# Performance work log

Measured on AMD Instinct MI355X. Metric: run time of the kernel, lower is better.

The kernel has to match this reference:

```python
import jax, jax.numpy as jnp
import numpy as np

N, E, F, H, L, STEPS, VH = 50000, 800000, 64, 64, 4, 4, 64
S1 = H * L + H          # 320
VIN = S1 + H            # 384
REG_IN = S1 + VH + 1    # 385
EPS = 1e-5


def setup_inputs() -> dict:
    key = jax.random.key(0)
    ks = iter(jax.random.split(key, 64))
    nk = lambda: next(ks)

    def w(shape):
        fan_in = shape[-2] if len(shape) > 1 else shape[-1]
        return jax.random.normal(nk(), shape, jnp.float32) / np.float32(np.sqrt(fan_in))

    def b(shape):
        return 0.01 * jax.random.normal(nk(), shape, jnp.float32)

    return {
        "x": jax.random.normal(nk(), (N, F), jnp.float32),
        "edge_index": jax.random.randint(nk(), (2, E), 0, N, jnp.int32),
        "W_in": w((F, H)), "b_in": b((H,)),
        # stacked per-layer SAGEConv params (all layers are H->H)
        "sage_Wl": w((L, H, H)), "sage_bl": b((L, H)), "sage_Wr": w((L, H, H)),
        "bn_gamma": jnp.ones((L, H), jnp.float32) + 0.1 * jax.random.normal(nk(), (L, H), jnp.float32),
        "bn_beta": b((L, H)),
        "bn_mean": 0.1 * jax.random.normal(nk(), (L, H), jnp.float32),
        "bn_var": 1.0 + 0.5 * jax.random.uniform(nk(), (L, H), jnp.float32),
        "vW_l": w((VIN, VH)), "vb_l": b((VH,)), "vW_r": w((VIN, VH)),
        "vbn_gamma": jnp.ones((VH,), jnp.float32) + 0.1 * jax.random.normal(nk(), (VH,), jnp.float32),
        "vbn_beta": b((VH,)),
        "vbn_mean": 0.1 * jax.random.normal(nk(), (VH,), jnp.float32),
        "vbn_var": 1.0 + 0.5 * jax.random.uniform(nk(), (VH,), jnp.float32),
        "W_mu": w((VH, VH)), "b_mu": b((VH,)),
        "W_lv": w((VH, VH)), "b_lv": b((VH,)),
        "rank_W1": w((VH, H)), "rank_b1": b((H,)),
        "rank_W2": w((H, 1)), "rank_b2": b((1,)),
        "reg_W1": w((REG_IN, H)), "reg_b1": b((H,)),
        "reg_W2": w((H, H // 2)), "reg_b2": b((H // 2,)),
        "reg_W3": w((H // 2, 1)), "reg_b3": b((1,)),
    }


def reference(x, edge_index, W_in, b_in, sage_Wl, sage_bl, sage_Wr,
              bn_gamma, bn_beta, bn_mean, bn_var,
              vW_l, vb_l, vW_r, vbn_gamma, vbn_beta, vbn_mean, vbn_var,
              W_mu, b_mu, W_lv, b_lv,
              rank_W1, rank_b1, rank_W2, rank_b2,
              reg_W1, reg_b1, reg_W2, reg_b2, reg_W3, reg_b3):
    n = x.shape[0]
    row, col = edge_index[0], edge_index[1]
    ones_e = jnp.ones(row.shape, x.dtype)

    def sage(h, Wl, bl, Wr):
        # mean aggregation of source features at destination nodes (PyG SAGEConv)
        agg = jax.ops.segment_sum(h[row], col, num_segments=n)          # [N, Fin]
        cnt = jax.ops.segment_sum(ones_e, col, num_segments=n)          # in-degree
        mean = agg / jnp.maximum(cnt, 1.0)[:, None]
        return mean @ Wl + bl + h @ Wr

    def bn(h, g, be, m, v):
        return (h - m) * jax.lax.rsqrt(v + EPS) * g + be

    inp_skip = x @ W_in + b_in
    h = x
    layer_outputs = []
    for i in range(L):  # fixed small layer loop; res_proj is Identity (in_feats == hidden)
        h_fwd = jax.nn.relu(bn(sage(h, sage_Wl[i], sage_bl[i], sage_Wr[i]),
                               bn_gamma[i], bn_beta[i], bn_mean[i], bn_var[i]))
        h = h_fwd + h
        layer_outputs.append(h)
    stage1 = jnp.concatenate(layer_outputs + [inp_skip], axis=1)        # [N, 320]

    # path_agg: row-degree-normalized scatter, iterated path_steps times
    deg = jnp.maximum(jax.ops.segment_sum(ones_e, row, num_segments=n), 1.0)
    norm = (1.0 / deg)[row]                                             # [E]
    out = h
    for _ in range(STEPS):
        out = jax.ops.segment_sum(out[row] * norm[:, None], col, num_segments=n)

    vgae_in = jnp.concatenate([stage1, out], axis=1)                    # [N, 384]
    v = jax.nn.relu(bn(sage(vgae_in, vW_l, vb_l, vW_r),
                       vbn_gamma, vbn_beta, vbn_mean, vbn_var))
    mu = v @ W_mu + b_mu
    logvar = v @ W_lv + b_lv
    z = mu  # eval mode: no reparameterization noise

    rank_score = (jax.nn.relu(z @ rank_W1 + rank_b1) @ rank_W2 + rank_b2)[:, 0]

    reg_in = jnp.concatenate([stage1, z, rank_score[:, None]], axis=1)  # [N, 385]
    h1 = jax.nn.relu(reg_in @ reg_W1 + reg_b1)
    h2 = jax.nn.relu(h1 @ reg_W2 + reg_b2)
    preds = h2 @ reg_W3 + reg_b3
    return preds, rank_score, mu, logvar
```

## Files before the change

### kernel.cpp

```cpp
#include <hip/hip_runtime.h>
#include <cstdint>
#include <cstddef>

#define NN 50000
#define EE 800000
#define CAP 64
#define EPS_BN 1e-5f

typedef short  s16x8 __attribute__((ext_vector_type(8)));
typedef ushort u16x8 __attribute__((ext_vector_type(8)));
typedef float  f32x4 __attribute__((ext_vector_type(4)));

#define MFMA16(a, b, c) __builtin_amdgcn_mfma_f32_16x16x32_bf16((a), (b), (c), 0, 0, 0)

__device__ inline ushort f2bf(float f){
  uint32_t u = __float_as_uint(f);
  uint32_t r = (u + 0x7FFFu + ((u >> 16) & 1u)) >> 16;
  return (ushort)r;
}
__device__ inline float bf2f(ushort u){ return __uint_as_float((uint32_t)u << 16); }


__global__ void k_outdeg(const int* __restrict__ row, int* __restrict__ outdeg){
  int e = blockIdx.x * blockDim.x + threadIdx.x;
  if (e < EE) atomicAdd(&outdeg[row[e]], 1);
}

__global__ void k_fill(const int* __restrict__ row, const int* __restrict__ col,
                       const int* __restrict__ outdeg,
                       int* __restrict__ incnt, int* __restrict__ bsrc,
                       float* __restrict__ bnorm){
  int e = blockIdx.x * blockDim.x + threadIdx.x;
  if (e >= EE) return;
  int r = row[e], c = col[e];
  int j = atomicAdd(&incnt[c], 1);
  if (j < CAP){
    bsrc[(size_t)c * CAP + j]  = r;
    bnorm[(size_t)c * CAP + j] = 1.0f / fmaxf((float)outdeg[r], 1.0f);
  }
}


__global__ void k_cvt(const float* __restrict__ src, ushort* __restrict__ dst, int n4){
  int i = blockIdx.x * blockDim.x + threadIdx.x;
  int stride = gridDim.x * blockDim.x;
  for (; i < n4; i += stride){
    float4 v = ((const float4*)src)[i];
    ushort4 u = {f2bf(v.x), f2bf(v.y), f2bf(v.z), f2bf(v.w)};
    ((ushort4*)dst)[i] = u;
  }
}


struct FJob { const float* srcA; const float* srcB; ushort* dst;
              int NF; int NCT; int P; int mode; int splitVal; };
struct FJobs { FJob j[10]; };

__global__ void k_conv(FJobs J){
  FJob jb = J.j[blockIdx.x];
  int total = jb.NCT * jb.P * 1024;
  for (int idx = threadIdx.x + blockIdx.y * 256; idx < total; idx += 256 * gridDim.y){
    int j = idx & 7, lane = (idx >> 3) & 63, ks = (idx >> 9) & 1;
    int rest = idx >> 10;
    int p = rest % jb.P, ct = rest / jb.P;
    int col = ct * 16 + (lane & 15);
    int k   = p * 64 + ks * 32 + (lane >> 4) * 8 + j;
    const float* s = jb.srcA;
    int sc = col, sk = k;
    if (jb.mode == 1 && k   >= jb.splitVal){ s = jb.srcB; sk = k   - jb.splitVal; }
    if (jb.mode == 2 && col >= jb.splitVal){ s = jb.srcB; sc = col - jb.splitVal; }
    jb.dst[idx] = f2bf(s[(size_t)sk * jb.NF + sc]);
  }
}


__global__ void __launch_bounds__(256) k_agg(const ushort* __restrict__ hin,
                                             ushort* __restrict__ out,
                                             const int* __restrict__ bsrc,
                                             const float* __restrict__ bnorm,
                                             const int* __restrict__ incnt,
                                             int use_norm){
  __shared__ int   sidx[4][CAP];
  __shared__ float swgt[4][CAP];
  int wib  = threadIdx.x >> 6;
  int lane = threadIdx.x & 63;
  int wid  = blockIdx.x * 4 + wib;
  bool valid = wid < NN;
  int cnt  = valid ? incnt[wid] : 0;
  int cntb = min(cnt, CAP);
  if (valid){
    int   si = (lane < cntb) ? bsrc[(size_t)wid * CAP + lane] : 0;
    float wv;
    if (use_norm) wv = (lane < cntb) ? bnorm[(size_t)wid * CAP + lane] : 0.f;
    else          wv = (lane < cntb) ? 1.0f / fmaxf((float)cnt, 1.f) : 0.f;
    sidx[wib][lane] = si;
    swgt[wib][lane] = wv;
  }
  __syncthreads();
  if (!valid) return;

  int g  = lane >> 3;
  int fl = lane & 7;
  float accf[8] = {0,0,0,0,0,0,0,0};
  for (int e0 = 0; e0 < cntb; e0 += 8){
    int e = e0 + g;
    int   s = sidx[wib][e];
    float w = swgt[wib][e];
    u16x8 v = *(const u16x8*)(hin + (size_t)s * 64 + fl * 8);
    #pragma unroll
    for (int j = 0; j < 8; ++j) accf[j] = fmaf(w, bf2f(v[j]), accf[j]);
  }
  #pragma unroll
  for (int m = 8; m < 64; m <<= 1){
    #pragma unroll
    for (int j = 0; j < 8; ++j) accf[j] += __shfl_xor(accf[j], m);
  }
  if (lane < 8){
    u16x8 o;
    #pragma unroll
    for (int j = 0; j < 8; ++j) o[j] = f2bf(accf[j]);
    *(u16x8*)(out + (size_t)wid * 64 + lane * 8) = o;
  }
}


template<int P, int NCT>
__device__ inline void gemm_direct(const ushort* const* pieces,
                                   const ushort* __restrict__ WB,
                                   int rowbase, f32x4* acc){
  int lane = threadIdx.x & 63;
  int q = lane >> 4, r16 = lane & 15;
  int ar = rowbase + r16; ar = (ar < NN) ? ar : (NN - 1);
  const ushort* wl = WB + lane * 8;
  #pragma unroll
  for (int p = 0; p < P; ++p){
    const ushort* src = pieces[p] + (size_t)ar * 64 + q * 8;
    #pragma unroll
    for (int ks = 0; ks < 2; ++ks){
      s16x8 a = *(const s16x8*)(src + ks * 32);
      #pragma unroll
      for (int ct = 0; ct < NCT; ++ct){
        s16x8 b = *(const s16x8*)(wl + (((ct * P + p) * 2 + ks) << 9));
        acc[ct] = MFMA16(a, b, acc[ct]);
      }
    }
  }
}

__global__ void __launch_bounds__(256) k_skip(const ushort* __restrict__ xb,
                                              const ushort* __restrict__ WT,
                                              const float* __restrict__ bias,
                                              ushort* __restrict__ outb){
  int lane = threadIdx.x & 63, wv = threadIdx.x >> 6, q = lane >> 4, r16 = lane & 15;
  int rowbase = blockIdx.x * 64 + wv * 16;
  const ushort* pieces[1] = {xb};
  f32x4 acc[4] = {};
  gemm_direct<1, 4>(pieces, WT, rowbase, acc);
  #pragma unroll
  for (int ct = 0; ct < 4; ++ct){
    int col = ct * 16 + r16;
    float b = bias[col];
    #pragma unroll
    for (int r = 0; r < 4; ++r){
      int row = rowbase + q * 4 + r;
      if (row < NN) outb[(size_t)row * 64 + col] = f2bf(acc[ct][r] + b);
    }
  }
}

__global__ void __launch_bounds__(256) k_sage_m(const ushort* __restrict__ meanb,
                                                const ushort* __restrict__ hb,
                                                const ushort* __restrict__ WT,
                                                const float* __restrict__ bl,
                                                const float* __restrict__ g,
                                                const float* __restrict__ be,
                                                const float* __restrict__ m_,
                                                const float* __restrict__ var_,
                                                ushort* __restrict__ houtb){
  int lane = threadIdx.x & 63, wv = threadIdx.x >> 6, q = lane >> 4, r16 = lane & 15;
  int rowbase = blockIdx.x * 64 + wv * 16;
  const ushort* pieces[2] = {meanb, hb};
  f32x4 acc[4] = {};
  gemm_direct<2, 4>(pieces, WT, rowbase, acc);
  #pragma unroll
  for (int ct = 0; ct < 4; ++ct){
    int col = ct * 16 + r16;
    float sc = g[col] * rsqrtf(var_[col] + EPS_BN);
    float sh = be[col] - m_[col] * sc;
    float bb = bl[col];
    #pragma unroll
    for (int r = 0; r < 4; ++r){
      int row = rowbase + q * 4 + r;
      if (row < NN){
        float t = (acc[ct][r] + bb) * sc + sh;
        float hv = bf2f(hb[(size_t)row * 64 + col]);
        houtb[(size_t)row * 64 + col] = f2bf(fmaxf(t, 0.f) + hv);
      }
    }
  }
}

__global__ void __launch_bounds__(256) k_yr(const ushort* __restrict__ x0, const ushort* __restrict__ x1,
                                            const ushort* __restrict__ x2, const ushort* __restrict__ x3,
                                            const ushort* __restrict__ x4, const ushort* __restrict__ x5,
                                            const ushort* __restrict__ WT, const float* __restrict__ vbl,
                                            ushort* __restrict__ Y, ushort* __restrict__ R){
  int lane = threadIdx.x & 63, wv = threadIdx.x >> 6, q = lane >> 4, r16 = lane & 15;
  int rowbase = blockIdx.x * 64 + wv * 16;
  const ushort* pieces[6] = {x0, x1, x2, x3, x4, x5};
  f32x4 acc[8] = {};
  gemm_direct<6, 8>(pieces, WT, rowbase, acc);
  #pragma unroll
  for (int ct = 0; ct < 8; ++ct){
    int col = ct * 16 + r16;
    bool isR = col >= 64;
    int c2 = isR ? (col - 64) : col;
    float b = isR ? vbl[c2] : 0.f;
    ushort* dst = isR ? R : Y;
    #pragma unroll
    for (int r = 0; r < 4; ++r){
      int row = rowbase + q * 4 + r;
      if (row < NN) dst[(size_t)row * 64 + c2] = f2bf(acc[ct][r] + b);
    }
  }
}

__global__ void __launch_bounds__(256) k_mulv_m(const ushort* __restrict__ Yagg,
                                                const ushort* __restrict__ Rb,
                                                const float* __restrict__ vg,
                                                const float* __restrict__ vbe,
                                                const float* __restrict__ vm,
                                                const float* __restrict__ vvar,
                                                const ushort* __restrict__ WT,
                                                const float* __restrict__ bmu,
                                                const float* __restrict__ blv,
                                                float* __restrict__ muf, float* __restrict__ lvf,
                                                ushort* __restrict__ mub){
  __shared__ float ssc[64], ssh[64];
  int t = threadIdx.x;
  if (t < 64){
    float sc = vg[t] * rsqrtf(vvar[t] + EPS_BN);
    ssc[t] = sc; ssh[t] = vbe[t] - vm[t] * sc;
  }
  __syncthreads();
  int lane = t & 63, wv = t >> 6, q = lane >> 4, r16 = lane & 15;
  int rowbase = blockIdx.x * 64 + wv * 16;
  int ar = rowbase + r16; ar = (ar < NN) ? ar : (NN - 1);
  const ushort* wl = WT + lane * 8;
  f32x4 acc[8] = {};
  #pragma unroll
  for (int ks = 0; ks < 2; ++ks){
    int k0 = ks * 32 + q * 8;
    u16x8 y  = *(const u16x8*)(Yagg + (size_t)ar * 64 + k0);
    u16x8 rv = *(const u16x8*)(Rb   + (size_t)ar * 64 + k0);
    s16x8 a;
    #pragma unroll
    for (int j = 0; j < 8; ++j){
      float tv = (bf2f(y[j]) + bf2f(rv[j])) * ssc[k0 + j] + ssh[k0 + j];
      a[j] = (short)f2bf(fmaxf(tv, 0.f));
    }
    #pragma unroll
    for (int ct = 0; ct < 8; ++ct){
      s16x8 b = *(const s16x8*)(wl + (((ct * 1) * 2 + ks) << 9));
      acc[ct] = MFMA16(a, b, acc[ct]);
    }
  }
  #pragma unroll
  for (int ct = 0; ct < 8; ++ct){
    int col = ct * 16 + r16;
    bool isL = col >= 64;
    int c2 = isL ? (col - 64) : col;
    float bb = isL ? blv[c2] : bmu[c2];
    #pragma unroll
    for (int r = 0; r < 4; ++r){
      int row = rowbase + q * 4 + r;
      if (row < NN){
        float v = acc[ct][r] + bb;
        if (isL) lvf[(size_t)row * 64 + c2] = v;
        else { muf[(size_t)row * 64 + c2] = v; mub[(size_t)row * 64 + c2] = f2bf(v); }
      }
    }
  }
}

__global__ void __launch_bounds__(256) k_rank_m(const ushort* __restrict__ mub,
                                                const ushort* __restrict__ WT,
                                                const float* __restrict__ rb1,
                                                const float* __restrict__ rW2,
                                                const float* __restrict__ rb2,
                                                float* __restrict__ rout){
  int lane = threadIdx.x & 63, wv = threadIdx.x >> 6, q = lane >> 4, r16 = lane & 15;
  int rowbase = blockIdx.x * 64 + wv * 16;
  const ushort* pieces[1] = {mub};
  f32x4 acc[4] = {};
  gemm_direct<1, 4>(pieces, WT, rowbase, acc);
  float val[4] = {0.f, 0.f, 0.f, 0.f};
  #pragma unroll
  for (int ct = 0; ct < 4; ++ct){
    int col = ct * 16 + r16;
    float b1 = rb1[col], w2 = rW2[col];
    #pragma unroll
    for (int r = 0; r < 4; ++r)
      val[r] += fmaxf(acc[ct][r] + b1, 0.f) * w2;
  }
  #pragma unroll
  for (int r = 0; r < 4; ++r){
    #pragma unroll
    for (int m = 1; m < 16; m <<= 1) val[r] += __shfl_xor(val[r], m);
  }
  if (r16 == 0){
    float b2 = rb2[0];
    #pragma unroll
    for (int r = 0; r < 4; ++r){
      int row = rowbase + q * 4 + r;
      if (row < NN) rout[row] = val[r] + b2;
    }
  }
}

__global__ void __launch_bounds__(256) k_reg1(const ushort* __restrict__ x0, const ushort* __restrict__ x1,
                                              const ushort* __restrict__ x2, const ushort* __restrict__ x3,
                                              const ushort* __restrict__ x4, const ushort* __restrict__ x5,
                                              const float* __restrict__ rank,
                                              const ushort* __restrict__ WT,
                                              const float* __restrict__ gW1,
                                              const float* __restrict__ gb1,
                                              ushort* __restrict__ h1b){
  int lane = threadIdx.x & 63, wv = threadIdx.x >> 6, q = lane >> 4, r16 = lane & 15;
  int rowbase = blockIdx.x * 64 + wv * 16;
  const ushort* pieces[6] = {x0, x1, x2, x3, x4, x5};
  f32x4 acc[4] = {};
  gemm_direct<6, 4>(pieces, WT, rowbase, acc);
  float rk[4];
  #pragma unroll
  for (int r = 0; r < 4; ++r){
    int row = rowbase + q * 4 + r;
    rk[r] = (row < NN) ? rank[row] : 0.f;
  }
  #pragma unroll
  for (int ct = 0; ct < 4; ++ct){
    int col = ct * 16 + r16;
    float b1 = gb1[col];
    float w384 = gW1[384 * 64 + col];
    #pragma unroll
    for (int r = 0; r < 4; ++r){
      int row = rowbase + q * 4 + r;
      if (row < NN)
        h1b[(size_t)row * 64 + col] = f2bf(fmaxf(acc[ct][r] + b1 + rk[r] * w384, 0.f));
    }
  }
}

__global__ void __launch_bounds__(256) k_reg2(const ushort* __restrict__ h1b,
                                              const ushort* __restrict__ WT,
                                              const float* __restrict__ gb2,
                                              const float* __restrict__ gW3,
                                              const float* __restrict__ gb3,
                                              float* __restrict__ preds){
  int lane = threadIdx.x & 63, wv = threadIdx.x >> 6, q = lane >> 4, r16 = lane & 15;
  int rowbase = blockIdx.x * 64 + wv * 16;
  const ushort* pieces[1] = {h1b};
  f32x4 acc[2] = {};
  gemm_direct<1, 2>(pieces, WT, rowbase, acc);
  float val[4] = {0.f, 0.f, 0.f, 0.f};
  #pragma unroll
  for (int ct = 0; ct < 2; ++ct){
    int col = ct * 16 + r16;
    float b2 = gb2[col], w3 = gW3[col];
    #pragma unroll
    for (int r = 0; r < 4; ++r)
      val[r] += fmaxf(acc[ct][r] + b2, 0.f) * w3;
  }
  #pragma unroll
  for (int r = 0; r < 4; ++r){
    #pragma unroll
    for (int m = 1; m < 16; m <<= 1) val[r] += __shfl_xor(val[r], m);
  }
  if (r16 == 0){
    float b3 = gb3[0];
    #pragma unroll
    for (int r = 0; r < 4; ++r){
      int row = rowbase + q * 4 + r;
      if (row < NN) preds[row] = val[r] + b3;
    }
  }
}


extern "C" void kernel_launch(void* const* d_in, const int* in_sizes, int n_in,
                              void* d_out, int out_size, void* d_ws, size_t ws_size,
                              hipStream_t stream){
  const float* x    = (const float*)d_in[0];
  const int*   eidx = (const int*)d_in[1];
  const int* row = eidx;
  const int* col = eidx + EE;
  const float* W_in = (const float*)d_in[2];
  const float* b_in = (const float*)d_in[3];
  const float* sWl  = (const float*)d_in[4];
  const float* sbl  = (const float*)d_in[5];
  const float* sWr  = (const float*)d_in[6];
  const float* bng  = (const float*)d_in[7];
  const float* bnb  = (const float*)d_in[8];
  const float* bnm  = (const float*)d_in[9];
  const float* bnv  = (const float*)d_in[10];
  const float* vWl  = (const float*)d_in[11];
  const float* vbl  = (const float*)d_in[12];
  const float* vWr  = (const float*)d_in[13];
  const float* vg   = (const float*)d_in[14];
  const float* vbe  = (const float*)d_in[15];
  const float* vm   = (const float*)d_in[16];
  const float* vvar = (const float*)d_in[17];
  const float* Wmu  = (const float*)d_in[18];
  const float* bmu  = (const float*)d_in[19];
  const float* Wlv  = (const float*)d_in[20];
  const float* blv  = (const float*)d_in[21];
  const float* rW1  = (const float*)d_in[22];
  const float* rb1  = (const float*)d_in[23];
  const float* rW2  = (const float*)d_in[24];
  const float* rb2  = (const float*)d_in[25];
  const float* gW1  = (const float*)d_in[26];
  const float* gb1  = (const float*)d_in[27];
  const float* gW2  = (const float*)d_in[28];
  const float* gb2  = (const float*)d_in[29];
  const float* gW3  = (const float*)d_in[30];
  const float* gb3  = (const float*)d_in[31];

  float* preds = (float*)d_out;
  float* rank  = preds + NN;
  float* mu    = rank + NN;
  float* lv    = mu + (size_t)NN * 64;

  char* w = (char*)d_ws;
  auto alloc = [&](size_t bytes) -> char* {
    char* p = w; w += (bytes + 255) & ~(size_t)255; return p;
  };
  int*   outdeg = (int*)alloc((size_t)NN * 4);
  int*   incnt  = (int*)alloc((size_t)NN * 4);
  int*   bsrc   = (int*)alloc((size_t)NN * CAP * 4);
  float* bnorm  = (float*)alloc((size_t)NN * CAP * 4);
  const size_t FB = (size_t)NN * 64 * 2;
  ushort* xb    = (ushort*)alloc(FB);
  ushort* skipb = (ushort*)alloc(FB);
  ushort* hb[4];
  for (int i = 0; i < 4; ++i) hb[i] = (ushort*)alloc(FB);
  ushort* meanb = (ushort*)alloc(FB);
  ushort* pa    = (ushort*)alloc(FB);
  ushort* pb    = (ushort*)alloc(FB);
  ushort* Yb    = (ushort*)alloc(FB);
  ushort* Rb    = (ushort*)alloc(FB);
  ushort* mub   = (ushort*)alloc(FB);
  ushort* skipW = (ushort*)alloc(4 * 1024 * 2);
  ushort* sageW = (ushort*)alloc(4 * 8 * 1024 * 2);
  ushort* yrW   = (ushort*)alloc(48 * 1024 * 2);
  ushort* mulvW = (ushort*)alloc(8 * 1024 * 2);
  ushort* rankW = (ushort*)alloc(4 * 1024 * 2);
  ushort* regW1 = (ushort*)alloc(24 * 1024 * 2);
  ushort* regW2 = (ushort*)alloc(2 * 1024 * 2);

  hipMemsetAsync(outdeg, 0, (size_t)NN * 4, stream);
  hipMemsetAsync(incnt,  0, (size_t)NN * 4, stream);

  const int EB = (EE + 255) / 256;
  k_outdeg<<<EB, 256, 0, stream>>>(row, outdeg);
  k_fill  <<<EB, 256, 0, stream>>>(row, col, outdeg, incnt, bsrc, bnorm);

  FJobs J;
  auto job = [&](int i, const float* sA, const float* sB, ushort* d,
                 int NF, int NCT, int P, int mode, int splitVal){
    J.j[i] = {sA, sB, d, NF, NCT, P, mode, splitVal};
  };
  job(0, W_in, nullptr, skipW, 64, 4, 1, 0, 0);
  for (int i = 0; i < 4; ++i)
    job(1 + i, sWl + i * 4096, sWr + i * 4096, sageW + i * 8192, 64, 4, 2, 1, 64);
  job(5, vWl, vWr, yrW,   64, 8, 6, 2, 64);
  job(6, Wmu, Wlv, mulvW, 64, 8, 1, 2, 64);
  job(7, rW1, nullptr, rankW, 64, 4, 1, 0, 0);
  job(8, gW1, nullptr, regW1, 64, 4, 6, 0, 0);
  job(9, gW2, nullptr, regW2, 32, 2, 1, 0, 0);
  k_conv<<<dim3(10, 8), 256, 0, stream>>>(J);

  k_cvt<<<1024, 256, 0, stream>>>(x, xb, NN * 64 / 4);

  const int GB = (NN + 63) / 64;
  k_skip<<<GB, 256, 0, stream>>>(xb, skipW, b_in, skipb);

  const int AGG_B = (NN + 3) / 4;
  const ushort* hprev = xb;
  for (int i = 0; i < 4; ++i){
    k_agg<<<AGG_B, 256, 0, stream>>>(hprev, meanb, bsrc, bnorm, incnt, 0);
    k_sage_m<<<GB, 256, 0, stream>>>(meanb, hprev, sageW + i * 8192, sbl + i * 64,
                                     bng + i * 64, bnb + i * 64, bnm + i * 64, bnv + i * 64, hb[i]);
    hprev = hb[i];
  }

  k_agg<<<AGG_B, 256, 0, stream>>>(hb[3], pa, bsrc, bnorm, incnt, 1);
  k_agg<<<AGG_B, 256, 0, stream>>>(pa, pb, bsrc, bnorm, incnt, 1);
  k_agg<<<AGG_B, 256, 0, stream>>>(pb, pa, bsrc, bnorm, incnt, 1);
  k_agg<<<AGG_B, 256, 0, stream>>>(pa, pb, bsrc, bnorm, incnt, 1);

  k_yr<<<GB, 256, 0, stream>>>(hb[0], hb[1], hb[2], hb[3], skipb, pb, yrW, vbl, Yb, Rb);
  k_agg<<<AGG_B, 256, 0, stream>>>(Yb, meanb, bsrc, bnorm, incnt, 0);
  k_mulv_m<<<GB, 256, 0, stream>>>(meanb, Rb, vg, vbe, vm, vvar, mulvW, bmu, blv, mu, lv, mub);
  k_rank_m<<<GB, 256, 0, stream>>>(mub, rankW, rb1, rW2, rb2, rank);
  k_reg1<<<GB, 256, 0, stream>>>(hb[0], hb[1], hb[2], hb[3], skipb, mub, rank,
                                 regW1, gW1, gb1, pa);
  k_reg2<<<GB, 256, 0, stream>>>(pa, regW2, gb2, gW3, gb3, preds);
}
```

Measured before the change: 539.2 us.

## Pack edge source and degree into one word; aggregate four nodes per wave

Edge buckets now store source index and out-degree packed in one 32-bit word instead of separate index and norm arrays, halving bucket metadata traffic; weights are recomputed from the packed degree. The aggregation kernel processes four destination nodes per wave with interleaved gathers, raising memory-level parallelism and removing the block barrier. It risks wasted work when neighbor counts differ within a group and relies on indices and degrees fitting in 16 bits.

```diff
diff --git a/kernel.cpp b/kernel.cpp
--- a/kernel.cpp
+++ b/kernel.cpp
@@ -28,16 +28,13 @@
 
 __global__ void k_fill(const int* __restrict__ row, const int* __restrict__ col,
                        const int* __restrict__ outdeg,
-                       int* __restrict__ incnt, int* __restrict__ bsrc,
-                       float* __restrict__ bnorm){
+                       int* __restrict__ incnt, uint* __restrict__ bpack){
   int e = blockIdx.x * blockDim.x + threadIdx.x;
   if (e >= EE) return;
   int r = row[e], c = col[e];
   int j = atomicAdd(&incnt[c], 1);
-  if (j < CAP){
-    bsrc[(size_t)c * CAP + j]  = r;
-    bnorm[(size_t)c * CAP + j] = 1.0f / fmaxf((float)outdeg[r], 1.0f);
-  }
+  if (j < CAP)
+    bpack[(size_t)c * CAP + j] = ((uint)outdeg[r] << 16) | (uint)r;
 }
 
 
@@ -76,50 +73,67 @@
 
 __global__ void __launch_bounds__(256) k_agg(const ushort* __restrict__ hin,
                                              ushort* __restrict__ out,
-                                             const int* __restrict__ bsrc,
-                                             const float* __restrict__ bnorm,
+                                             const uint* __restrict__ bpack,
                                              const int* __restrict__ incnt,
                                              int use_norm){
-  __shared__ int   sidx[4][CAP];
-  __shared__ float swgt[4][CAP];
+  __shared__ int   ssrc[4][4][CAP];
+  __shared__ float swgt[4][4][CAP];
   int wib  = threadIdx.x >> 6;
   int lane = threadIdx.x & 63;
-  int wid  = blockIdx.x * 4 + wib;
-  bool valid = wid < NN;
-  int cnt  = valid ? incnt[wid] : 0;
-  int cntb = min(cnt, CAP);
-  if (valid){
-    int   si = (lane < cntb) ? bsrc[(size_t)wid * CAP + lane] : 0;
-    float wv;
-    if (use_norm) wv = (lane < cntb) ? bnorm[(size_t)wid * CAP + lane] : 0.f;
-    else          wv = (lane < cntb) ? 1.0f / fmaxf((float)cnt, 1.f) : 0.f;
-    sidx[wib][lane] = si;
-    swgt[wib][lane] = wv;
-  }
-  __syncthreads();
-  if (!valid) return;
-
-  int g  = lane >> 3;
-  int fl = lane & 7;
-  float accf[8] = {0,0,0,0,0,0,0,0};
-  for (int e0 = 0; e0 < cntb; e0 += 8){
+  int n0   = (blockIdx.x * 4 + wib) * 4;
+  int g = lane >> 3, fl = lane & 7;
+
+  int cm[4];
+  #pragma unroll
+  for (int ni = 0; ni < 4; ++ni){
+    int node = n0 + ni;
+    bool v = node < NN;
+    int cnt  = v ? incnt[node] : 0;
+    int cntb = min(cnt, CAP);
+    cm[ni] = cntb;
+    uint pk = (v && lane < cntb) ? bpack[(size_t)node * CAP + lane] : 0u;
+    float w = 0.f;
+    if (lane < cntb){
+      float deg = (float)(pk >> 16);
+      w = use_norm ? 1.0f / fmaxf(deg, 1.f) : 1.0f / fmaxf((float)cnt, 1.f);
+    }
+    ssrc[wib][ni][lane] = (int)(pk & 0xFFFFu);
+    swgt[wib][ni][lane] = w;
+  }
+  int maxc = max(max(cm[0], cm[1]), max(cm[2], cm[3]));
+
+  float acc[4][8];
+  #pragma unroll
+  for (int ni = 0; ni < 4; ++ni)
+    #pragma unroll
+    for (int j = 0; j < 8; ++j) acc[ni][j] = 0.f;
+
+  for (int e0 = 0; e0 < maxc; e0 += 8){
     int e = e0 + g;
-    int   s = sidx[wib][e];
-    float w = swgt[wib][e];
-    u16x8 v = *(const u16x8*)(hin + (size_t)s * 64 + fl * 8);
-    #pragma unroll
-    for (int j = 0; j < 8; ++j) accf[j] = fmaf(w, bf2f(v[j]), accf[j]);
-  }
-  #pragma unroll
-  for (int m = 8; m < 64; m <<= 1){
-    #pragma unroll
-    for (int j = 0; j < 8; ++j) accf[j] += __shfl_xor(accf[j], m);
-  }
-  if (lane < 8){
-    u16x8 o;
-    #pragma unroll
-    for (int j = 0; j < 8; ++j) o[j] = f2bf(accf[j]);
-    *(u16x8*)(out + (size_t)wid * 64 + lane * 8) = o;
+    #pragma unroll
+    for (int ni = 0; ni < 4; ++ni){
+      int   s = ssrc[wib][ni][e];
+      float w = swgt[wib][ni][e];
+      u16x8 v = *(const u16x8*)(hin + (size_t)s * 64 + fl * 8);
+      #pragma unroll
+      for (int j = 0; j < 8; ++j) acc[ni][j] = fmaf(w, bf2f(v[j]), acc[ni][j]);
+    }
+  }
+
+  #pragma unroll
+  for (int ni = 0; ni < 4; ++ni){
+    #pragma unroll
+    for (int m = 8; m < 64; m <<= 1){
+      #pragma unroll
+      for (int j = 0; j < 8; ++j) acc[ni][j] += __shfl_xor(acc[ni][j], m);
+    }
+    int node = n0 + ni;
+    if (node < NN && lane < 8){
+      u16x8 o;
+      #pragma unroll
+      for (int j = 0; j < 8; ++j) o[j] = f2bf(acc[ni][j]);
+      *(u16x8*)(out + (size_t)node * 64 + lane * 8) = o;
+    }
   }
 }
 
@@ -436,8 +450,7 @@
   };
   int*   outdeg = (int*)alloc((size_t)NN * 4);
   int*   incnt  = (int*)alloc((size_t)NN * 4);
-  int*   bsrc   = (int*)alloc((size_t)NN * CAP * 4);
-  float* bnorm  = (float*)alloc((size_t)NN * CAP * 4);
+  uint*  bpack  = (uint*)alloc((size_t)NN * CAP * 4);
   const size_t FB = (size_t)NN * 64 * 2;
   ushort* xb    = (ushort*)alloc(FB);
   ushort* skipb = (ushort*)alloc(FB);
@@ -462,7 +475,7 @@
 
   const int EB = (EE + 255) / 256;
   k_outdeg<<<EB, 256, 0, stream>>>(row, outdeg);
-  k_fill  <<<EB, 256, 0, stream>>>(row, col, outdeg, incnt, bsrc, bnorm);
+  k_fill  <<<EB, 256, 0, stream>>>(row, col, outdeg, incnt, bpack);
 
   FJobs J;
   auto job = [&](int i, const float* sA, const float* sB, ushort* d,
@@ -484,22 +497,22 @@
   const int GB = (NN + 63) / 64;
   k_skip<<<GB, 256, 0, stream>>>(xb, skipW, b_in, skipb);
 
-  const int AGG_B = (NN + 3) / 4;
+  const int AGG_B = (NN + 15) / 16;
   const ushort* hprev = xb;
   for (int i = 0; i < 4; ++i){
-    k_agg<<<AGG_B, 256, 0, stream>>>(hprev, meanb, bsrc, bnorm, incnt, 0);
+    k_agg<<<AGG_B, 256, 0, stream>>>(hprev, meanb, bpack, incnt, 0);
     k_sage_m<<<GB, 256, 0, stream>>>(meanb, hprev, sageW + i * 8192, sbl + i * 64,
                                      bng + i * 64, bnb + i * 64, bnm + i * 64, bnv + i * 64, hb[i]);
     hprev = hb[i];
   }
 
-  k_agg<<<AGG_B, 256, 0, stream>>>(hb[3], pa, bsrc, bnorm, incnt, 1);
-  k_agg<<<AGG_B, 256, 0, stream>>>(pa, pb, bsrc, bnorm, incnt, 1);
-  k_agg<<<AGG_B, 256, 0, stream>>>(pb, pa, bsrc, bnorm, incnt, 1);
-  k_agg<<<AGG_B, 256, 0, stream>>>(pa, pb, bsrc, bnorm, incnt, 1);
+  k_agg<<<AGG_B, 256, 0, stream>>>(hb[3], pa, bpack, incnt, 1);
+  k_agg<<<AGG_B, 256, 0, stream>>>(pa, pb, bpack, incnt, 1);
+  k_agg<<<AGG_B, 256, 0, stream>>>(pb, pa, bpack, incnt, 1);
+  k_agg<<<AGG_B, 256, 0, stream>>>(pa, pb, bpack, incnt, 1);
 
   k_yr<<<GB, 256, 0, stream>>>(hb[0], hb[1], hb[2], hb[3], skipb, pb, yrW, vbl, Yb, Rb);
-  k_agg<<<AGG_B, 256, 0, stream>>>(Yb, meanb, bsrc, bnorm, incnt, 0);
+  k_agg<<<AGG_B, 256, 0, stream>>>(Yb, meanb, bpack, incnt, 0);
   k_mulv_m<<<GB, 256, 0, stream>>>(meanb, Rb, vg, vbe, vm, vvar, mulvW, bmu, blv, mu, lv, mub);
   k_rank_m<<<GB, 256, 0, stream>>>(mub, rankW, rb1, rW2, rb2, rank);
   k_reg1<<<GB, 256, 0, stream>>>(hb[0], hb[1], hb[2], hb[3], skipb, mub, rank,
```

New measurement: 569.4 us. 5.6% more time.

## Compact neighbor lists to 16-bit indices, per-node inverse degree, unroll aggregation by two

Applied to the files above, without the earlier changes.

Neighbor source indices are now stored as 16-bit values, since N is below 65536. The per-edge normalization array is replaced by a per-node inverse-degree array, computed once in a new small kernel and gathered inside the aggregation kernel. The aggregation loop now processes two edges per lane group per iteration, with zero-padded shared slots so the extra edges read harmlessly. The intent is less memory traffic in the bucket build and in the nine aggregation passes, plus more memory-level parallelism. The cost is an extra random gather of invdeg and a hard dependence on N fitting in 16 bits.

```diff
diff --git a/kernel.cpp b/kernel.cpp
--- a/kernel.cpp
+++ b/kernel.cpp
@@ -26,18 +26,18 @@
   if (e < EE) atomicAdd(&outdeg[row[e]], 1);
 }
 
+__global__ void k_invdeg(const int* __restrict__ outdeg, float* __restrict__ invdeg){
+  int n = blockIdx.x * blockDim.x + threadIdx.x;
+  if (n < NN) invdeg[n] = 1.0f / fmaxf((float)outdeg[n], 1.0f);
+}
+
 __global__ void k_fill(const int* __restrict__ row, const int* __restrict__ col,
-                       const int* __restrict__ outdeg,
-                       int* __restrict__ incnt, int* __restrict__ bsrc,
-                       float* __restrict__ bnorm){
+                       int* __restrict__ incnt, ushort* __restrict__ bsrc16){
   int e = blockIdx.x * blockDim.x + threadIdx.x;
   if (e >= EE) return;
   int r = row[e], c = col[e];
   int j = atomicAdd(&incnt[c], 1);
-  if (j < CAP){
-    bsrc[(size_t)c * CAP + j]  = r;
-    bnorm[(size_t)c * CAP + j] = 1.0f / fmaxf((float)outdeg[r], 1.0f);
-  }
+  if (j < CAP) bsrc16[(size_t)c * CAP + j] = (ushort)r;
 }
 
 
@@ -76,12 +76,12 @@
 
 __global__ void __launch_bounds__(256) k_agg(const ushort* __restrict__ hin,
                                              ushort* __restrict__ out,
-                                             const int* __restrict__ bsrc,
-                                             const float* __restrict__ bnorm,
+                                             const ushort* __restrict__ bsrc16,
+                                             const float* __restrict__ invdeg,
                                              const int* __restrict__ incnt,
                                              int use_norm){
-  __shared__ int   sidx[4][CAP];
-  __shared__ float swgt[4][CAP];
+  __shared__ int   sidx[4][CAP + 16];
+  __shared__ float swgt[4][CAP + 16];
   int wib  = threadIdx.x >> 6;
   int lane = threadIdx.x & 63;
   int wid  = blockIdx.x * 4 + wib;
@@ -89,12 +89,13 @@
   int cnt  = valid ? incnt[wid] : 0;
   int cntb = min(cnt, CAP);
   if (valid){
-    int   si = (lane < cntb) ? bsrc[(size_t)wid * CAP + lane] : 0;
-    float wv;
-    if (use_norm) wv = (lane < cntb) ? bnorm[(size_t)wid * CAP + lane] : 0.f;
-    else          wv = (lane < cntb) ? 1.0f / fmaxf((float)cnt, 1.f) : 0.f;
-    sidx[wib][lane] = si;
-    swgt[wib][lane] = wv;
+    int src = (lane < cntb) ? (int)bsrc16[(size_t)wid * CAP + lane] : 0;
+    float w = 0.f;
+    if (lane < cntb)
+      w = use_norm ? invdeg[src] : (1.0f / fmaxf((float)cnt, 1.f));
+    sidx[wib][lane] = src;
+    swgt[wib][lane] = w;
+    if (lane < 16){ sidx[wib][CAP + lane] = 0; swgt[wib][CAP + lane] = 0.f; }
   }
   __syncthreads();
   if (!valid) return;
@@ -102,13 +103,17 @@
   int g  = lane >> 3;
   int fl = lane & 7;
   float accf[8] = {0,0,0,0,0,0,0,0};
-  for (int e0 = 0; e0 < cntb; e0 += 8){
-    int e = e0 + g;
-    int   s = sidx[wib][e];
-    float w = swgt[wib][e];
-    u16x8 v = *(const u16x8*)(hin + (size_t)s * 64 + fl * 8);
-    #pragma unroll
-    for (int j = 0; j < 8; ++j) accf[j] = fmaf(w, bf2f(v[j]), accf[j]);
+  for (int e0 = 0; e0 < cntb; e0 += 16){
+    int ea = e0 + g, eb = e0 + g + 8;
+    int   sa = sidx[wib][ea], sb = sidx[wib][eb];
+    float wa = swgt[wib][ea], wb = swgt[wib][eb];
+    u16x8 va = *(const u16x8*)(hin + (size_t)sa * 64 + fl * 8);
+    u16x8 vb = *(const u16x8*)(hin + (size_t)sb * 64 + fl * 8);
+    #pragma unroll
+    for (int j = 0; j < 8; ++j){
+      accf[j] = fmaf(wa, bf2f(va[j]), accf[j]);
+      accf[j] = fmaf(wb, bf2f(vb[j]), accf[j]);
+    }
   }
   #pragma unroll
   for (int m = 8; m < 64; m <<= 1){
@@ -434,10 +439,10 @@
   auto alloc = [&](size_t bytes) -> char* {
     char* p = w; w += (bytes + 255) & ~(size_t)255; return p;
   };
-  int*   outdeg = (int*)alloc((size_t)NN * 4);
-  int*   incnt  = (int*)alloc((size_t)NN * 4);
-  int*   bsrc   = (int*)alloc((size_t)NN * CAP * 4);
-  float* bnorm  = (float*)alloc((size_t)NN * CAP * 4);
+  int*    outdeg = (int*)alloc((size_t)NN * 4);
+  int*    incnt  = (int*)alloc((size_t)NN * 4);
+  float*  invdeg = (float*)alloc((size_t)NN * 4);
+  ushort* bsrc16 = (ushort*)alloc((size_t)NN * CAP * 2);
   const size_t FB = (size_t)NN * 64 * 2;
   ushort* xb    = (ushort*)alloc(FB);
   ushort* skipb = (ushort*)alloc(FB);
@@ -462,7 +467,8 @@
 
   const int EB = (EE + 255) / 256;
   k_outdeg<<<EB, 256, 0, stream>>>(row, outdeg);
-  k_fill  <<<EB, 256, 0, stream>>>(row, col, outdeg, incnt, bsrc, bnorm);
+  k_invdeg<<<(NN + 255) / 256, 256, 0, stream>>>(outdeg, invdeg);
+  k_fill  <<<EB, 256, 0, stream>>>(row, col, incnt, bsrc16);
 
   FJobs J;
   auto job = [&](int i, const float* sA, const float* sB, ushort* d,
@@ -487,19 +493,19 @@
   const int AGG_B = (NN + 3) / 4;
   const ushort* hprev = xb;
   for (int i = 0; i < 4; ++i){
-    k_agg<<<AGG_B, 256, 0, stream>>>(hprev, meanb, bsrc, bnorm, incnt, 0);
+    k_agg<<<AGG_B, 256, 0, stream>>>(hprev, meanb, bsrc16, invdeg, incnt, 0);
     k_sage_m<<<GB, 256, 0, stream>>>(meanb, hprev, sageW + i * 8192, sbl + i * 64,
                                      bng + i * 64, bnb + i * 64, bnm + i * 64, bnv + i * 64, hb[i]);
     hprev = hb[i];
   }
 
-  k_agg<<<AGG_B, 256, 0, stream>>>(hb[3], pa, bsrc, bnorm, incnt, 1);
-  k_agg<<<AGG_B, 256, 0, stream>>>(pa, pb, bsrc, bnorm, incnt, 1);
-  k_agg<<<AGG_B, 256, 0, stream>>>(pb, pa, bsrc, bnorm, incnt, 1);
-  k_agg<<<AGG_B, 256, 0, stream>>>(pa, pb, bsrc, bnorm, incnt, 1);
+  k_agg<<<AGG_B, 256, 0, stream>>>(hb[3], pa, bsrc16, invdeg, incnt, 1);
+  k_agg<<<AGG_B, 256, 0, stream>>>(pa, pb, bsrc16, invdeg, incnt, 1);
+  k_agg<<<AGG_B, 256, 0, stream>>>(pb, pa, bsrc16, invdeg, incnt, 1);
+  k_agg<<<AGG_B, 256, 0, stream>>>(pa, pb, bsrc16, invdeg, incnt, 1);
 
   k_yr<<<GB, 256, 0, stream>>>(hb[0], hb[1], hb[2], hb[3], skipb, pb, yrW, vbl, Yb, Rb);
-  k_agg<<<AGG_B, 256, 0, stream>>>(Yb, meanb, bsrc, bnorm, incnt, 0);
+  k_agg<<<AGG_B, 256, 0, stream>>>(Yb, meanb, bsrc16, invdeg, incnt, 0);
   k_mulv_m<<<GB, 256, 0, stream>>>(meanb, Rb, vg, vbe, vm, vvar, mulvW, bmu, blv, mu, lv, mub);
   k_rank_m<<<GB, 256, 0, stream>>>(mub, rankW, rb1, rW2, rb2, rank);
   k_reg1<<<GB, 256, 0, stream>>>(hb[0], hb[1], hb[2], hb[3], skipb, mub, rank,
```

Result: no change. 529.0 us (-1.9%).
